# Kernel tuning notes

Hardware: AMD Instinct MI355X
Metric: run time of the kernel (lower is better)

The kernel has to match this reference:

```python
import jax, jax.numpy as jnp
import numpy as np
import math

B, S, D, H = 2, 2048, 1024, 16
DH = D // H

def setup_inputs() -> dict:
    key0 = jax.random.key(0)
    ks = jax.random.split(key0, 12)
    s = 1.0 / math.sqrt(D)
    return {
        "query": jax.random.normal(ks[0], (B, S, D), jnp.float32),
        "key": jax.random.normal(ks[1], (B, S, D), jnp.float32),
        "value": jax.random.normal(ks[2], (B, S, D), jnp.float32),
        "mask": jax.random.randint(ks[3], (B, 1, S, S), 0, 2, jnp.int32),
        "Wq": jax.random.normal(ks[4], (D, D), jnp.float32) * s,
        "bq": jnp.zeros((D,), jnp.float32),
        "Wk": jax.random.normal(ks[5], (D, D), jnp.float32) * s,
        "bk": jnp.zeros((D,), jnp.float32),
        "Wv": jax.random.normal(ks[6], (D, D), jnp.float32) * s,
        "bv": jnp.zeros((D,), jnp.float32),
        "Wo": jax.random.normal(ks[7], (D, D), jnp.float32) * s,
        "bo": jnp.zeros((D,), jnp.float32),
    }

def reference(query, key, value, mask, Wq, bq, Wk, bk, Wv, bv, Wo, bo):
    # Linear projections (torch Linear: x @ W.T + b)
    q = query @ Wq.T + bq
    k = key @ Wk.T + bk
    v = value @ Wv.T + bv
    # [B, S, D] -> [B, H, S, DH]
    q = q.reshape(B, S, H, DH).transpose(0, 2, 1, 3)
    k = k.reshape(B, S, H, DH).transpose(0, 2, 1, 3)
    v = v.reshape(B, S, H, DH).transpose(0, 2, 1, 3)
    # scaled dot-product attention with explicit [B,H,S,S] scores
    score = jnp.einsum('bhqd,bhkd->bhqk', q, k) / math.sqrt(DH)
    score = jnp.where(mask == 0, jnp.float32(-1e9), score)
    attn = jax.nn.softmax(score, axis=-1)
    out = jnp.einsum('bhqk,bhkd->bhqd', attn, v)
    out = out.transpose(0, 2, 1, 3).reshape(B, S, D)
    return out @ Wo.T + bo
```

## Files before the change

### kernel.cpp

```cpp
#include <hip/hip_runtime.h>
#include <hip/hip_bf16.h>

typedef __attribute__((ext_vector_type(4))) float f32x4;
typedef __attribute__((ext_vector_type(8))) short bf16x8;
typedef __attribute__((ext_vector_type(4))) short s16x4;
typedef __attribute__((ext_vector_type(4))) unsigned int u32x4;
typedef unsigned short ushort_t;
typedef unsigned int u32;
typedef unsigned long long u64;

constexpr int B = 2, S = 2048, D = 1024, H = 16, DH = 64;

__device__ __forceinline__ ushort_t f2bf(float f) {
    union { float f; unsigned int i; } v; v.f = f;
    unsigned int r = v.i + 0x7fffu + ((v.i >> 16) & 1u);
    return (ushort_t)(r >> 16);
}

__device__ __forceinline__ float fast_exp2(float x) {
#if __has_builtin(__builtin_amdgcn_exp2f)
    return __builtin_amdgcn_exp2f(x);
#else
    return exp2f(x);
#endif
}

__device__ __forceinline__ u32 pack_hi16(u32 b1, u32 b0) {
#if __has_builtin(__builtin_amdgcn_perm)
    return __builtin_amdgcn_perm(b1, b0, 0x07060302u);
#else
    return (b1 & 0xffff0000u) | (b0 >> 16);
#endif
}

__device__ __forceinline__ void gload_lds16(const void* g, void* l) {
    __builtin_amdgcn_global_load_lds(
        (const __attribute__((address_space(1))) unsigned int*)g,
        (__attribute__((address_space(3))) unsigned int*)l,
        16, 0, 0);
}

__global__ __launch_bounds__(256) void cvt_f32_bf16(
    const float* __restrict__ in, ushort_t* __restrict__ out, int n)
{
    int i = (blockIdx.x * 256 + threadIdx.x) * 4;
    if (i >= n) return;
    f32x4 v = *(const f32x4*)(in + i);
    s16x4 o;
    for (int j = 0; j < 4; ++j) o[j] = (short)f2bf(v[j]);
    *(s16x4*)(out + i) = o;
}

__global__ __launch_bounds__(256) void prep_all(
    const float* __restrict__ qin, const float* __restrict__ kin,
    const float* __restrict__ vin,
    const float* __restrict__ wq, const float* __restrict__ wk,
    const float* __restrict__ wv, const float* __restrict__ wo,
    const int* __restrict__ mask,
    ushort_t* __restrict__ X3, ushort_t* __restrict__ W4,
    u64* __restrict__ pm, int nx, int nw)
{
    const int y = blockIdx.y;
    if (y < 3) {
        const float* in = y == 0 ? qin : (y == 1 ? kin : vin);
        int i = (blockIdx.x * 256 + threadIdx.x) * 4;
        if (i >= nx) return;
        f32x4 v = *(const f32x4*)(in + i);
        s16x4 o;
        #pragma unroll
        for (int j = 0; j < 4; ++j) o[j] = (short)f2bf(v[j]);
        *(s16x4*)(X3 + (size_t)y * nx + i) = o;
    } else if (y == 3) {
        int wsel = blockIdx.x >> 10;
        int xb = blockIdx.x & 1023;
        const float* in = wsel == 0 ? wq : (wsel == 1 ? wk :
                          (wsel == 2 ? wv : wo));
        int i = (xb * 256 + threadIdx.x) * 4;
        if (i >= nw) return;
        f32x4 v = *(const f32x4*)(in + i);
        s16x4 o;
        #pragma unroll
        for (int j = 0; j < 4; ++j) o[j] = (short)f2bf(v[j]);
        *(s16x4*)(W4 + (size_t)wsel * nw + i) = o;
    } else {
        if (blockIdx.x >= 2048) return;
        const int wave_g = (blockIdx.x * 256 + threadIdx.x) >> 6;
        const int lane = threadIdx.x & 63;
        for (int w = 0; w < 16; ++w) {
            size_t idx = (size_t)wave_g * 16 + w;
            int mv = mask[idx * 64 + lane];
            u64 bal = __ballot(mv != 0);
            if (lane == 0) {
                int t = (int)(idx & 31);
                int q = (int)((idx >> 5) & (S - 1));
                int b = (int)(idx >> 16);
                pm[((size_t)b * 32 + t) * S + q] = bal;
            }
        }
    }
}

__global__ __launch_bounds__(256) void pack_mask(
    const int* __restrict__ mask, u64* __restrict__ pm)
{
    const int wave_g = (blockIdx.x * 256 + threadIdx.x) >> 6;
    const int lane = threadIdx.x & 63;
    for (int w = 0; w < 16; ++w) {
        size_t idx = (size_t)wave_g * 16 + w;
        int mv = mask[idx * 64 + lane];
        u64 bal = __ballot(mv != 0);
        if (lane == 0) {
            int t = (int)(idx & 31);
            int q = (int)((idx >> 5) & (S - 1));
            int b = (int)(idx >> 16);
            pm[((size_t)b * 32 + t) * S + q] = bal;
        }
    }
}

__global__ __launch_bounds__(256) void transpose_v(
    const ushort_t* __restrict__ Vw, ushort_t* __restrict__ Vt)
{
    __shared__ ushort_t T[64][80];
    const int st = blockIdx.x, bh = blockIdx.y;
    const int b = bh / H, h = bh % H;
    const int tid = threadIdx.x;
    const int r = tid >> 3, c = tid & 7;
    for (int p = 0; p < 2; ++p) {
        int s = p * 32 + r;
        bf16x8 v = *(const bf16x8*)(Vw + (size_t)(b * S + st * 64 + s) * D + h * DH + c * 8);
        *(bf16x8*)(&T[s][c * 8]) = v;
    }
    __syncthreads();
    const int q0q = (c >> 2) * 8 + (c & 3);
    for (int p = 0; p < 2; ++p) {
        int d = p * 32 + r;
        bf16x8 o;
        for (int j = 0; j < 4; ++j) o[j]     = (short)T[q0q * 4 + j][d];
        for (int j = 0; j < 4; ++j) o[4 + j] = (short)T[(q0q + 4) * 4 + j][d];
        *(bf16x8*)(Vt + (size_t)((b * H + h) * DH + d) * S + st * 64 + c * 8) = o;
    }
}

template <typename OutT>
__device__ __forceinline__ void gemm_body128(
    const ushort_t* __restrict__ Ag,
    const ushort_t* __restrict__ Wg,
    const float* __restrict__ bias,
    OutT* __restrict__ Cg,
    ushort_t* __restrict__ VtOut,
    int M, int N, int K,
    ushort_t* SH, bool vepi)
{
    constexpr int BK = 64;
    ushort_t* As = SH;
    ushort_t* Bs = SH + 128 * 64;
    const int tid  = threadIdx.x;
    const int wid  = tid >> 6;
    const int lane = tid & 63;
    const int m0 = blockIdx.x * 128;
    const int n0 = blockIdx.y * 128;
    const int wr = wid >> 1, wc = wid & 1;

    const int lrow = lane & 15;
    const int lk8  = (lane >> 4) * 8;
    const int srow  = lane >> 3;
    const int sbyte = (lane & 7) * 16;

    f32x4 acc[4][4] = {};

    for (int k0 = 0; k0 < K; k0 += BK) {
        #pragma unroll
        for (int c = 0; c < 4; ++c) {
            int r0 = wid * 32 + c * 8;
            gload_lds16((const char*)(Ag + (size_t)(m0 + r0 + srow) * K + k0) + sbyte,
                        (char*)As + r0 * 128);
            gload_lds16((const char*)(Wg + (size_t)(n0 + r0 + srow) * K + k0) + sbyte,
                        (char*)Bs + r0 * 128);
        }
        __syncthreads();

        #pragma unroll
        for (int kk = 0; kk < BK; kk += 32) {
            bf16x8 af[4], bfr[4];
            #pragma unroll
            for (int i = 0; i < 4; ++i) {
                af[i]  = *(const bf16x8*)(As + (wr * 64 + i * 16 + lrow) * BK + kk + lk8);
                bfr[i] = *(const bf16x8*)(Bs + (wc * 64 + i * 16 + lrow) * BK + kk + lk8);
            }
            #pragma unroll
            for (int i = 0; i < 4; ++i)
                #pragma unroll
                for (int j = 0; j < 4; ++j)
                    acc[i][j] = __builtin_amdgcn_mfma_f32_16x16x32_bf16(
                        af[i], bfr[j], acc[i][j], 0, 0, 0);
        }
        __syncthreads();
    }

    const int hi    = lane >> 4;
    const int crow0 = hi * 4;
    const int ccol  = lane & 15;

    if (vepi) {
        #pragma unroll
        for (int j = 0; j < 4; ++j) {
            int dl = wc * 64 + j * 16 + ccol;
            float bv = bias[n0 + dl];
            #pragma unroll
            for (int i = 0; i < 4; ++i) {
                int pos = wr * 64 + ((i >> 1) * 4 + hi) * 8 + (i & 1) * 4;
                s16x4 o;
                #pragma unroll
                for (int r = 0; r < 4; ++r) o[r] = (short)f2bf(acc[i][j][r] + bv);
                *(s16x4*)(SH + dl * 132 + pos) = o;
            }
        }
        __syncthreads();
        const int b = m0 >> 11;
        const int sbase = m0 & (S - 1);
        #pragma unroll
        for (int rr = 0; rr < 32; ++rr) {
            int dl = wid * 32 + rr;
            int dg = n0 + dl;
            u32 w2 = *(const u32*)(SH + dl * 132 + lane * 2);
            *(u32*)(VtOut + ((size_t)(b * H + (dg >> 6)) * DH + (dg & 63)) * S
                    + sbase + lane * 2) = w2;
        }
    } else {
        #pragma unroll
        for (int j = 0; j < 4; ++j) {
            int col = n0 + wc * 64 + j * 16 + ccol;
            float bv = bias[col];
            #pragma unroll
            for (int i = 0; i < 4; ++i) {
                #pragma unroll
                for (int r = 0; r < 4; ++r) {
                    int row = m0 + wr * 64 + i * 16 + crow0 + r;
                    float val = acc[i][j][r] + bv;
                    if constexpr (__is_same(OutT, float))
                        Cg[(size_t)row * N + col] = val;
                    else
                        Cg[(size_t)row * N + col] = f2bf(val);
                }
            }
        }
    }
}

template <typename OutT>
__device__ __forceinline__ void gemm_body64(
    const ushort_t* __restrict__ Ag,
    const ushort_t* __restrict__ Wg,
    const float* __restrict__ bias,
    OutT* __restrict__ Cg,
    int M, int N, int K,
    ushort_t* As, ushort_t* Bs)
{
    constexpr int BK = 64;
    const int tid  = threadIdx.x;
    const int wid  = tid >> 6;
    const int lane = tid & 63;
    const int m0 = blockIdx.x * 128;
    const int n0 = blockIdx.y * 64;
    const int wr = wid >> 1, wc = wid & 1;

    const int lrow = lane & 15;
    const int lk8  = (lane >> 4) * 8;
    const int srow  = lane >> 3;
    const int sbyte = (lane & 7) * 16;

    f32x4 acc[4][2] = {};

    for (int k0 = 0; k0 < K; k0 += BK) {
        #pragma unroll
        for (int c = 0; c < 4; ++c) {
            int r0 = wid * 32 + c * 8;
            gload_lds16((const char*)(Ag + (size_t)(m0 + r0 + srow) * K + k0) + sbyte,
                        (char*)As + r0 * 128);
        }
        #pragma unroll
        for (int c = 0; c < 2; ++c) {
            int r0 = wid * 16 + c * 8;
            gload_lds16((const char*)(Wg + (size_t)(n0 + r0 + srow) * K + k0) + sbyte,
                        (char*)Bs + r0 * 128);
        }
        __syncthreads();

        #pragma unroll
        for (int kk = 0; kk < BK; kk += 32) {
            bf16x8 af[4], bfr[2];
            #pragma unroll
            for (int i = 0; i < 4; ++i)
                af[i]  = *(const bf16x8*)(As + (wr * 64 + i * 16 + lrow) * BK + kk + lk8);
            #pragma unroll
            for (int j = 0; j < 2; ++j)
                bfr[j] = *(const bf16x8*)(Bs + (wc * 32 + j * 16 + lrow) * BK + kk + lk8);
            #pragma unroll
            for (int i = 0; i < 4; ++i)
                #pragma unroll
                for (int j = 0; j < 2; ++j)
                    acc[i][j] = __builtin_amdgcn_mfma_f32_16x16x32_bf16(
                        af[i], bfr[j], acc[i][j], 0, 0, 0);
        }
        __syncthreads();
    }

    const int crow0 = (lane >> 4) * 4;
    const int ccol  = lane & 15;
    #pragma unroll
    for (int j = 0; j < 2; ++j) {
        int col = n0 + wc * 32 + j * 16 + ccol;
        float bv = bias[col];
        #pragma unroll
        for (int i = 0; i < 4; ++i) {
            #pragma unroll
            for (int r = 0; r < 4; ++r) {
                int row = m0 + wr * 64 + i * 16 + crow0 + r;
                float val = acc[i][j][r] + bv;
                if constexpr (__is_same(OutT, float))
                    Cg[(size_t)row * N + col] = val;
                else
                    Cg[(size_t)row * N + col] = f2bf(val);
            }
        }
    }
}

template <typename OutT>
__global__ __launch_bounds__(256, 4) void gemm_bt_bias(
    const ushort_t* __restrict__ Ag, const ushort_t* __restrict__ Wg,
    const float* __restrict__ bias, OutT* __restrict__ Cg,
    int M, int N, int K)
{
    __shared__ ushort_t As[128 * 64];
    __shared__ ushort_t Bs[64 * 64];
    gemm_body64<OutT>(Ag, Wg, bias, Cg, M, N, K, As, Bs);
}

__global__ __launch_bounds__(256, 2) void gemm_qkv(
    const ushort_t* __restrict__ X3,
    const ushort_t* __restrict__ W4,
    const float* __restrict__ b0, const float* __restrict__ b1,
    const float* __restrict__ b2,
    ushort_t* __restrict__ QKV,
    ushort_t* __restrict__ Vt,
    int M, int N, int K)
{
    __shared__ ushort_t SH[128 * 132];
    const int z = blockIdx.z;
    const float* bias = z == 0 ? b0 : (z == 1 ? b1 : b2);
    gemm_body128<ushort_t>(X3 + (size_t)z * M * K, W4 + (size_t)z * N * K,
                           bias, QKV + (size_t)z * M * N, Vt,
                           M, N, K, SH, z == 2);
}

__global__ __launch_bounds__(256, 4) void attn_kernel(
    const ushort_t* __restrict__ Q,
    const ushort_t* __restrict__ Kt,
    const ushort_t* __restrict__ Vt,
    const u64* __restrict__ pmask,
    ushort_t* __restrict__ O)
{
    constexpr int NT2 = S / 128;
    constexpr float C1 = 0.18033688f;
    constexpr float C2 = 17.31234049f;
    __shared__ ushort_t Ks[2][64 * DH];
    __shared__ ushort_t Vs[2][64 * DH];

    const int tid  = threadIdx.x;
    const int wid  = tid >> 6;
    const int lane = tid & 63;
    const int bid = blockIdx.x + 32 * blockIdx.y;
    const int j8  = bid >> 3;
    const int bh  = (bid & 7) * 4 + (j8 >> 5);
    const int qt  = j8 & 31;
    const int b = bh / H, h = bh % H;
    const int q0 = qt * 64 + wid * 16;

    const int lq   = lane & 15;
    const int hi   = lane >> 4;
    const int lk8  = hi * 8;
    const int srow = lane >> 3;
    const int sbyte = (((lane & 7) ^ srow) & 7) * 16;

    bf16x8 qf[2];
    #pragma unroll
    for (int kk = 0; kk < 2; ++kk)
        qf[kk] = *(const bf16x8*)(Q + (size_t)(b * S + q0 + lq) * D + h * DH + kk * 32 + lk8);

    f32x4 oacc[4] = {};
    f32x4 ps = {};
    const u32x4 onesw = {0x3f803f80u, 0x3f803f80u, 0x3f803f80u, 0x3f803f80u};
    const bf16x8 onesf = __builtin_bit_cast(bf16x8, onesw);

    const u64* pmrow = pmask + (size_t)b * 32 * S + q0 + lq;
    const ushort_t* Vtb = Vt + (size_t)(b * H + h) * DH * S;

    auto compute = [&](const ushort_t* Kc, const ushort_t* Vc, u64 mw) {
        f32x4 sc[4] = {};
        #pragma unroll
        for (int kk = 0; kk < 2; ++kk) {
            const int chunk = ((kk * 4 + hi) ^ (lq & 7)) * 8;
            #pragma unroll
            for (int ni = 0; ni < 4; ++ni) {
                bf16x8 kf = *(const bf16x8*)(Kc + (ni * 16 + lq) * 64 + chunk);
                sc[ni] = __builtin_amdgcn_mfma_f32_16x16x32_bf16(kf, qf[kk], sc[ni], 0, 0, 0);
            }
        }
        const u32 lo32 = (u32)mw;
        const u32 hi32 = (u32)(mw >> 32);
        u32 paw[8];
        #pragma unroll
        for (int ni = 0; ni < 4; ++ni) {
            const u32 word = (ni < 2) ? lo32 : hi32;
            const int base = (ni & 1) * 16 + hi * 4;
            u32 pb[4];
            #pragma unroll
            for (int r = 0; r < 4; ++r) {
                float p = fast_exp2(__builtin_fmaf(sc[ni][r], C1, -C2));
                int mbit = ((int)(word << (31 - (base + r)))) >> 31;
                pb[r] = __builtin_bit_cast(u32, p) & (u32)mbit;
            }
            paw[ni * 2]     = pack_hi16(pb[1], pb[0]);
            paw[ni * 2 + 1] = pack_hi16(pb[3], pb[2]);
        }
        #pragma unroll
        for (int kk = 0; kk < 2; ++kk) {
            u32x4 pv = {paw[kk * 4], paw[kk * 4 + 1], paw[kk * 4 + 2], paw[kk * 4 + 3]};
            bf16x8 paf = __builtin_bit_cast(bf16x8, pv);
            ps = __builtin_amdgcn_mfma_f32_16x16x32_bf16(paf, onesf, ps, 0, 0, 0);
            const int chunk = ((kk * 4 + hi) ^ (lq & 7)) * 8;
            #pragma unroll
            for (int di = 0; di < 4; ++di) {
                bf16x8 vf = *(const bf16x8*)(Vc + (di * 16 + lq) * 64 + chunk);
                oacc[di] = __builtin_amdgcn_mfma_f32_16x16x32_bf16(paf, vf, oacc[di], 0, 0, 0);
            }
        }
    };

    for (int t = 0; t < NT2; ++t) {
        #pragma unroll
        for (int half = 0; half < 2; ++half) {
            const int kv0 = (t * 2 + half) * 64;
            #pragma unroll
            for (int c = 0; c < 2; ++c) {
                int r0 = wid * 16 + c * 8;
                gload_lds16((const char*)(Kt + (size_t)(b * S + kv0 + r0 + srow) * D + h * DH) + sbyte,
                            (char*)Ks[half] + r0 * 128);
                gload_lds16((const char*)(Vtb + (size_t)(r0 + srow) * S + kv0) + sbyte,
                            (char*)Vs[half] + r0 * 128);
            }
        }
        const u64 mwa = pmrow[(size_t)(t * 2) * S];
        const u64 mwb = pmrow[(size_t)(t * 2 + 1) * S];
        __syncthreads();

        compute(Ks[0], Vs[0], mwa);
        compute(Ks[1], Vs[1], mwb);
        __syncthreads();
    }

    float inv[4];
    #pragma unroll
    for (int r = 0; r < 4; ++r) inv[r] = 1.0f / ps[r];
    #pragma unroll
    for (int di = 0; di < 4; ++di) {
        #pragma unroll
        for (int r = 0; r < 4; ++r) {
            float v = oacc[di][r] * inv[r];
            O[(size_t)(b * S + q0 + hi * 4 + r) * D + h * DH + di * 16 + lq] = f2bf(v);
        }
    }
}

extern "C" void kernel_launch(void* const* d_in, const int* in_sizes, int n_in,
                              void* d_out, int out_size, void* d_ws, size_t ws_size,
                              hipStream_t stream) {
    const float* query = (const float*)d_in[0];
    const float* key   = (const float*)d_in[1];
    const float* value = (const float*)d_in[2];
    const int*   mask  = (const int*)d_in[3];
    const float* Wq = (const float*)d_in[4];
    const float* bq = (const float*)d_in[5];
    const float* Wk = (const float*)d_in[6];
    const float* bk = (const float*)d_in[7];
    const float* Wv = (const float*)d_in[8];
    const float* bv = (const float*)d_in[9];
    const float* Wo = (const float*)d_in[10];
    const float* bo = (const float*)d_in[11];
    float* out = (float*)d_out;

    const int M = B * S;
    const int NX = M * D;
    const int NW = D * D;

    char* ws = (char*)d_ws;
    const size_t MB = 1024 * 1024;
    dim3 gblk64(M / 128, D / 64);
    const int gcX = NX / (4 * 256);
    const int gcW = NW / (4 * 256);
    const int pmBlocks = (B * S * (S / 64)) / (16 * 4);

    if (ws_size >= 58 * MB) {
        ushort_t* X3  = (ushort_t*)(ws);
        ushort_t* Ow  = (ushort_t*)(ws + 8 * MB);
        ushort_t* W4  = (ushort_t*)(ws + 24 * MB);
        ushort_t* QKV = (ushort_t*)(ws + 32 * MB);
        ushort_t* Qw = QKV, *Kw = QKV + NX;
        ushort_t* Vtb = QKV + 2 * (size_t)NX;
        u64* pm = (u64*)(ws + 56 * MB);

        prep_all<<<dim3(gcX, 5), 256, 0, stream>>>(
            query, key, value, Wq, Wk, Wv, Wo, mask, X3, W4, pm, NX, NW);

        gemm_qkv<<<dim3(M / 128, D / 128, 3), 256, 0, stream>>>(
            X3, W4, bq, bk, bv, QKV, Vtb, M, D, D);

        attn_kernel<<<dim3(S / 64, B * H), 256, 0, stream>>>(Qw, Kw, Vtb, pm, Ow);

        gemm_bt_bias<float><<<gblk64, 256, 0, stream>>>(Ow, W4 + 3 * (size_t)NW, bo, out, M, D, D);
    } else {
        ushort_t* Xb = (ushort_t*)(ws);
        ushort_t* Vtb = (ushort_t*)(ws);
        ushort_t* Wb = (ushort_t*)(ws + 8  * MB);
        u64*      pm = (u64*)(ws + 8 * MB);
        ushort_t* Qw = (ushort_t*)(ws + 16 * MB);
        ushort_t* Kw = (ushort_t*)(ws + 24 * MB);
        ushort_t* Vw = (ushort_t*)(ws + 32 * MB);
        ushort_t* Ow = (ushort_t*)(ws + 40 * MB);

        cvt_f32_bf16<<<gcX, 256, 0, stream>>>(query, Xb, NX);
        cvt_f32_bf16<<<gcW, 256, 0, stream>>>(Wq, Wb, NW);
        gemm_bt_bias<ushort_t><<<gblk64, 256, 0, stream>>>(Xb, Wb, bq, Qw, M, D, D);

        cvt_f32_bf16<<<gcX, 256, 0, stream>>>(key, Xb, NX);
        cvt_f32_bf16<<<gcW, 256, 0, stream>>>(Wk, Wb, NW);
        gemm_bt_bias<ushort_t><<<gblk64, 256, 0, stream>>>(Xb, Wb, bk, Kw, M, D, D);

        cvt_f32_bf16<<<gcX, 256, 0, stream>>>(value, Xb, NX);
        cvt_f32_bf16<<<gcW, 256, 0, stream>>>(Wv, Wb, NW);
        gemm_bt_bias<ushort_t><<<gblk64, 256, 0, stream>>>(Xb, Wb, bv, Vw, M, D, D);

        transpose_v<<<dim3(S / 64, B * H), 256, 0, stream>>>(Vw, Vtb);
        pack_mask<<<pmBlocks, 256, 0, stream>>>(mask, pm);

        attn_kernel<<<dim3(S / 64, B * H), 256, 0, stream>>>(Qw, Kw, Vtb, pm, Ow);

        cvt_f32_bf16<<<gcW, 256, 0, stream>>>(Wo, Wb, NW);
        gemm_bt_bias<float><<<gblk64, 256, 0, stream>>>(Ow, Wb, bo, out, M, D, D);
    }
}
```

Before: 135.3 us.

## Double-buffer LDS tiles in QKV and output projection GEMMs

Both GEMM bodies now use two LDS buffers and issue the global-to-LDS loads for the next K tile before computing on the current one. A single waitcnt plus barrier per iteration replaces the two __syncthreads, so memory latency can overlap with MFMA work. LDS use grows to 64KB for the QKV kernel and 48KB for the output GEMM, which may reduce how many blocks fit per CU.

```diff
diff --git a/kernel.cpp b/kernel.cpp
--- a/kernel.cpp
+++ b/kernel.cpp
@@ -153,8 +153,6 @@
     ushort_t* SH, bool vepi)
 {
     constexpr int BK = 64;
-    ushort_t* As = SH;
-    ushort_t* Bs = SH + 128 * 64;
     const int tid  = threadIdx.x;
     const int wid  = tid >> 6;
     const int lane = tid & 63;
@@ -169,7 +167,9 @@
 
     f32x4 acc[4][4] = {};
 
-    for (int k0 = 0; k0 < K; k0 += BK) {
+    auto stage = [&](int k0, int buf) {
+        ushort_t* As = SH + buf * 16384;
+        ushort_t* Bs = As + 8192;
         #pragma unroll
         for (int c = 0; c < 4; ++c) {
             int r0 = wid * 32 + c * 8;
@@ -178,8 +178,18 @@
             gload_lds16((const char*)(Wg + (size_t)(n0 + r0 + srow) * K + k0) + sbyte,
                         (char*)Bs + r0 * 128);
         }
-        __syncthreads();
-
+    };
+
+    stage(0, 0);
+    asm volatile("s_waitcnt vmcnt(0)" ::: "memory");
+    __builtin_amdgcn_s_barrier();
+
+    int cur = 0;
+    for (int k0 = 0; k0 < K; k0 += BK) {
+        if (k0 + BK < K) stage(k0 + BK, cur ^ 1);
+
+        const ushort_t* As = SH + cur * 16384;
+        const ushort_t* Bs = As + 8192;
         #pragma unroll
         for (int kk = 0; kk < BK; kk += 32) {
             bf16x8 af[4], bfr[4];
@@ -195,7 +205,10 @@
                     acc[i][j] = __builtin_amdgcn_mfma_f32_16x16x32_bf16(
                         af[i], bfr[j], acc[i][j], 0, 0, 0);
         }
-        __syncthreads();
+
+        asm volatile("s_waitcnt vmcnt(0)" ::: "memory");
+        __builtin_amdgcn_s_barrier();
+        cur ^= 1;
     }
 
     const int hi    = lane >> 4;
@@ -255,7 +268,7 @@
     const float* __restrict__ bias,
     OutT* __restrict__ Cg,
     int M, int N, int K,
-    ushort_t* As, ushort_t* Bs)
+    ushort_t* SH)
 {
     constexpr int BK = 64;
     const int tid  = threadIdx.x;
@@ -272,7 +285,9 @@
 
     f32x4 acc[4][2] = {};
 
-    for (int k0 = 0; k0 < K; k0 += BK) {
+    auto stage = [&](int k0, int buf) {
+        ushort_t* As = SH + buf * 12288;
+        ushort_t* Bs = As + 8192;
         #pragma unroll
         for (int c = 0; c < 4; ++c) {
             int r0 = wid * 32 + c * 8;
@@ -285,8 +300,18 @@
             gload_lds16((const char*)(Wg + (size_t)(n0 + r0 + srow) * K + k0) + sbyte,
                         (char*)Bs + r0 * 128);
         }
-        __syncthreads();
-
+    };
+
+    stage(0, 0);
+    asm volatile("s_waitcnt vmcnt(0)" ::: "memory");
+    __builtin_amdgcn_s_barrier();
+
+    int cur = 0;
+    for (int k0 = 0; k0 < K; k0 += BK) {
+        if (k0 + BK < K) stage(k0 + BK, cur ^ 1);
+
+        const ushort_t* As = SH + cur * 12288;
+        const ushort_t* Bs = As + 8192;
         #pragma unroll
         for (int kk = 0; kk < BK; kk += 32) {
             bf16x8 af[4], bfr[2];
@@ -303,7 +328,10 @@
                     acc[i][j] = __builtin_amdgcn_mfma_f32_16x16x32_bf16(
                         af[i], bfr[j], acc[i][j], 0, 0, 0);
         }
-        __syncthreads();
+
+        asm volatile("s_waitcnt vmcnt(0)" ::: "memory");
+        __builtin_amdgcn_s_barrier();
+        cur ^= 1;
     }
 
     const int crow0 = (lane >> 4) * 4;
@@ -333,9 +361,8 @@
     const float* __restrict__ bias, OutT* __restrict__ Cg,
     int M, int N, int K)
 {
-    __shared__ ushort_t As[128 * 64];
-    __shared__ ushort_t Bs[64 * 64];
-    gemm_body64<OutT>(Ag, Wg, bias, Cg, M, N, K, As, Bs);
+    __shared__ ushort_t SH[24576];
+    gemm_body64<OutT>(Ag, Wg, bias, Cg, M, N, K, SH);
 }
 
 __global__ __launch_bounds__(256, 2) void gemm_qkv(
@@ -347,7 +374,7 @@
     ushort_t* __restrict__ Vt,
     int M, int N, int K)
 {
-    __shared__ ushort_t SH[128 * 132];
+    __shared__ ushort_t SH[32768];
     const int z = blockIdx.z;
     const float* bias = z == 0 ? b0 : (z == 1 ? b1 : b2);
     gemm_body128<ushort_t>(X3 + (size_t)z * M * K, W4 + (size_t)z * N * K,
```

Result: faster. 132.2 us (-2.3%).
